# Kernel optimization log

Hardware: AMD Instinct MI355X
Metric: run time of the kernel (lower is better)

## Reference

```python
import jax, jax.numpy as jnp
import numpy as np

B, T, DI, D = 8, 256, 64, 128
PRED_LEN, OUT_DIM = 96, 7
LN_EPS = 1e-5


def setup_inputs() -> dict:
    key = jax.random.key(0)
    ks = jax.random.split(key, 10)
    s = lambda k, shape, sc: (jax.random.normal(k, shape, jnp.float32) * sc)
    return {
        'x': s(ks[0], (B, T, DI), 1.0),
        'W_b': s(ks[1], (DI, D), DI ** -0.5), 'b_b': jnp.zeros((D,), jnp.float32),
        'Wk': s(ks[2], (D, D), D ** -0.5),
        'Wv': s(ks[3], (D, D), D ** -0.5),
        'Wq': s(ks[4], (D, D), D ** -0.5),
        'W_m': s(ks[5], (D, 3), D ** -0.5), 'b_m': jnp.zeros((3,), jnp.float32),
        'W_f': s(ks[6], (2 * D, D), (2 * D) ** -0.5), 'b_f': jnp.zeros((D,), jnp.float32),
        'W1': s(ks[7], (D, D), D ** -0.5), 'b1': jnp.zeros((D,), jnp.float32),
        'g1': jnp.ones((D,), jnp.float32), 'be1': jnp.zeros((D,), jnp.float32),
        'W2': s(ks[8], (D, PRED_LEN * OUT_DIM), D ** -0.5),
        'b2': jnp.zeros((PRED_LEN * OUT_DIM,), jnp.float32),
    }


def _layernorm(h, g, b):
    mu = h.mean(-1, keepdims=True)
    var = jnp.mean((h - mu) ** 2, -1, keepdims=True)
    return (h - mu) * jax.lax.rsqrt(var + LN_EPS) * g + b


def _forward(x, W_b, b_b, Wk, Wv, Wq, W_m, b_m, W_f, b_f, W1, b1, g1, be1, W2, b2):
    # Backbone P: feature extraction -> f_t  [B,T,D]
    f = jax.nn.gelu(x @ W_b + b_b)
    # Meta-learner: per-step (theta_t, eta_t, alpha_t)
    meta = jax.nn.sigmoid(f @ W_m + b_m)               # [B,T,3]
    theta = 0.01 * meta[..., 0]                         # learning rate
    eta = meta[..., 1]                                  # momentum
    alpha = 0.1 * meta[..., 2]                          # forget/decay
    # Key/value/query projections (precomputed; recurrence is in M,S only)
    k = f @ Wk; v = f @ Wv; q = f @ Wq                  # [B,T,D] each
    seq = (jnp.swapaxes(k, 0, 1), jnp.swapaxes(v, 0, 1), jnp.swapaxes(q, 0, 1),
           theta.T, eta.T, alpha.T)                     # time-major
    M0 = jnp.zeros((B, D, D), f.dtype)
    S0 = jnp.zeros((B, D, D), f.dtype)

    def step(carry, inp):
        M, S = carry
        kt, vt, qt, th, et, al = inp
        # grad of 0.5*||M k - v||^2 wrt M  (rank-1 outer product)
        err = jnp.einsum('bij,bj->bi', M, kt) - vt
        grad = jnp.einsum('bi,bj->bij', err, kt)
        S = et[:, None, None] * S - th[:, None, None] * grad
        M = (1.0 - al)[:, None, None] * M + S
        m_t = jnp.einsum('bij,bj->bi', M, qt)           # retrieve
        return (M, S), m_t

    (_, _), m_seq = jax.lax.scan(step, (M0, S0), seq)
    m = jnp.swapaxes(m_seq, 0, 1)                       # [B,T,D]
    # Gated fusion
    gate = jax.nn.sigmoid(jnp.concatenate([f, m], -1) @ W_f + b_f)
    fused = f * gate + m * (1.0 - gate)
    # Prediction head on last timestep (dropout=0 / eval)
    last = fused[:, -1, :]
    h = jax.nn.gelu(_layernorm(last @ W1 + b1, g1, be1))
    out = h @ W2 + b2
    return out.reshape(B, PRED_LEN, OUT_DIM)


def reference(x, W_b, b_b, Wk, Wv, Wq, W_m, b_m, W_f, b_f, W1, b1, g1, be1, W2, b2):
    return _forward(x, W_b, b_b, Wk, Wv, Wq, W_m, b_m, W_f, b_f, W1, b1, g1, be1, W2, b2)
```

## Files before the change

kernel.cpp:

```cpp
#include <hip/hip_runtime.h>
#include <hip/hip_bf16.h>

#define BB 8
#define TT 256
#define DIN 64
#define DD 128

__device__ __forceinline__ float gelu_tanh(float x) {
  float x3 = x * x * x;
  return 0.5f * x * (1.0f + tanhf(0.7978845608028654f * (x + 0.044715f * x3)));
}
__device__ __forceinline__ float sigmoidf(float x) {
  return 1.0f / (1.0f + __expf(-x));
}

template <typename T> __device__ __forceinline__ float getv(const void* p, int i);
template <> __device__ __forceinline__ float getv<float>(const void* p, int i) {
  return ((const float*)p)[i];
}
template <> __device__ __forceinline__ float getv<__hip_bfloat16>(const void* p, int i) {
  return __bfloat162float(((const __hip_bfloat16*)p)[i]);
}

template <int CTRL>
__device__ __forceinline__ float dpp_add(float x) {
  int s = __builtin_amdgcn_update_dpp(0, __float_as_int(x), CTRL, 0xF, 0xF, true);
  return x + __int_as_float(s);
}

__device__ __forceinline__ float rowsum16(float p) {
  p = dpp_add<0xB1>(p);
  p = dpp_add<0x4E>(p);
  p = dpp_add<0x124>(p);
  p = dpp_add<0x128>(p);
  return p;
}

__device__ __forceinline__ void gload_lds16(const void* g, void* l) {
  __builtin_amdgcn_global_load_lds(
      (const __attribute__((address_space(1))) void*)g,
      (__attribute__((address_space(3))) void*)l, 16, 0, 0);
}

__global__ void k0_detect(const void* x, int* flag) {
  __shared__ int cnt;
  if (threadIdx.x == 0) cnt = 0;
  __syncthreads();
  const unsigned short* u = (const unsigned short*)x;
  int good = 0;
  for (int idx = threadIdx.x; idx < 2048; idx += 256) {
    unsigned int bits = ((unsigned int)u[idx]) << 16;
    float f = __uint_as_float(bits);
    float a = fabsf(f);
    if (a == 0.0f || (a > 1e-4f && a < 100.0f)) good++;
  }
  atomicAdd(&cnt, good);
  __syncthreads();
  if (threadIdx.x == 0) *flag = (cnt >= 1536) ? 1 : 0;
}

template <typename T>
__device__ void k1_body(const void* x, const void* W_b, const void* b_b,
                        const void* Wk, const void* Wv, const void* Wq,
                        const void* W_m, const void* b_m,
                        float* kout, float* vout, float* scal4,
                        float* q_last, float* f_last) {
  const int row = blockIdx.x;
  const int b = row >> 8, t = row & 255;
  const int tid = threadIdx.x;
  __shared__ float xs[DIN];
  __shared__ float fs[DD];
  if (tid < DIN) xs[tid] = getv<T>(x, row * DIN + tid);
  __syncthreads();

  float acc = getv<T>(b_b, tid);
#pragma unroll 8
  for (int d = 0; d < DIN; ++d) acc += xs[d] * getv<T>(W_b, d * DD + tid);
  float f = gelu_tanh(acc);
  fs[tid] = f;
  __syncthreads();

  float ak = 0.0f, av = 0.0f;
#pragma unroll 8
  for (int c = 0; c < DD; ++c) {
    float fc = fs[c];
    ak += fc * getv<T>(Wk, c * DD + tid);
    av += fc * getv<T>(Wv, c * DD + tid);
  }
  kout[row * DD + tid] = ak;
  vout[row * DD + tid] = av;

  if (t == TT - 1) {
    float aq = 0.0f;
#pragma unroll 8
    for (int c = 0; c < DD; ++c) aq += fs[c] * getv<T>(Wq, c * DD + tid);
    q_last[b * DD + tid] = aq;
    f_last[b * DD + tid] = f;
  }
  if (tid < 4) {
    float val = 0.0f;
    if (tid < 3) {
      float a = getv<T>(b_m, tid);
      for (int c = 0; c < DD; ++c) a += fs[c] * getv<T>(W_m, c * 3 + tid);
      float s = sigmoidf(a);
      val = (tid == 0) ? 0.01f * s : ((tid == 1) ? s : 0.1f * s);
    }
    scal4[row * 4 + tid] = val;
  }
}

__global__ __launch_bounds__(128) void k1_kern(
    const void* x, const void* W_b, const void* b_b, const void* Wk,
    const void* Wv, const void* Wq, const void* W_m, const void* b_m,
    const int* flag, float* kout, float* vout, float* scal4, float* q_last,
    float* f_last) {
  if (*flag)
    k1_body<__hip_bfloat16>(x, W_b, b_b, Wk, Wv, Wq, W_m, b_m, kout, vout,
                            scal4, q_last, f_last);
  else
    k1_body<float>(x, W_b, b_b, Wk, Wv, Wq, W_m, b_m, kout, vout, scal4,
                   q_last, f_last);
}

__global__ __launch_bounds__(64) void k2_scan(
    const float* __restrict__ kbuf, const float* __restrict__ vbuf,
    const float* __restrict__ scal, const float* __restrict__ q_last,
    float* __restrict__ m_last) {
  const int tid = threadIdx.x;
  const int g = tid & 15;
  const int cidx = tid >> 4;
  const int chain = blockIdx.x * 4 + cidx;
  const int b = chain >> 7;
  const int i = chain & 127;
  const int i0 = (blockIdx.x * 4) & 127;

  __shared__ float kl[2][32 * DD];
  __shared__ float vl[TT * 4];
  __shared__ float4 scl[TT];

  const float* kslice = kbuf + (size_t)b * TT * DD;
  const float* vslice = vbuf + (size_t)b * TT * DD;

  for (int idx = tid; idx < TT * 4; idx += 64)
    vl[idx] = vslice[(idx >> 2) * DD + i0 + (idx & 3)];
  const float4* sp4 = (const float4*)scal + b * TT;
  for (int idx = tid; idx < TT; idx += 64) scl[idx] = sp4[idx];

#define K2_GLL(CH, BUF)                                                      \
  {                                                                          \
    const float* gs = kslice + (CH) * 32 * DD + tid * 4;                     \
    _Pragma("unroll") for (int j = 0; j < 16; ++j)                           \
        gload_lds16(gs + j * 256, &kl[BUF][j * 256]);                        \
  }
  K2_GLL(0, 0);

  float4 Ma = {0, 0, 0, 0}, Mb = {0, 0, 0, 0};
  float4 Sa = {0, 0, 0, 0}, Sb = {0, 0, 0, 0};

#define K2_STEP(KA, KB, VV, SC)                                              \
  {                                                                          \
    float p = (Ma.x * KA.x + Ma.y * KA.y) + (Ma.z * KA.z + Ma.w * KA.w) +    \
              (Mb.x * KB.x + Mb.y * KB.y) + (Mb.z * KB.z + Mb.w * KB.w);     \
    p = rowsum16(p);                                                         \
    const float err = p - VV;                                                \
    const float c = SC.x * err;                             \
    const float et = SC.y;                                          \
    const float am = 1.0f - SC.z;                             \
    Sa.x = et * Sa.x - c * KA.x;  Ma.x = am * Ma.x + Sa.x;                   \
    Sa.y = et * Sa.y - c * KA.y;  Ma.y = am * Ma.y + Sa.y;                   \
    Sa.z = et * Sa.z - c * KA.z;  Ma.z = am * Ma.z + Sa.z;                   \
    Sa.w = et * Sa.w - c * KA.w;  Ma.w = am * Ma.w + Sa.w;                   \
    Sb.x = et * Sb.x - c * KB.x;  Mb.x = am * Mb.x + Sb.x;                   \
    Sb.y = et * Sb.y - c * KB.y;  Mb.y = am * Mb.y + Sb.y;                   \
    Sb.z = et * Sb.z - c * KB.z;  Mb.z = am * Mb.z + Sb.z;                   \
    Sb.w = et * Sb.w - c * KB.w;  Mb.w = am * Mb.w + Sb.w;                   \
  }

  for (int ch = 0; ch < 8; ++ch) {
    asm volatile("s_waitcnt vmcnt(0) lgkmcnt(0)" ::: "memory");
    if (ch < 7) K2_GLL(ch + 1, (ch + 1) & 1);

    const float* kc = &kl[ch & 1][0];
    const int tbase = ch * 32;

    float4 ka = *(const float4*)(kc + g * 8);
    float4 kb = *(const float4*)(kc + g * 8 + 4);
    float vv = vl[tbase * 4 + cidx];
    float4 sc = scl[tbase];

#pragma unroll
    for (int tt = 0; tt < 32; ++tt) {
      float4 nka, nkb, nsc;
      float nv;
      if (tt < 31) {
        nka = *(const float4*)(kc + (tt + 1) * DD + g * 8);
        nkb = *(const float4*)(kc + (tt + 1) * DD + g * 8 + 4);
        nv = vl[(tbase + tt + 1) * 4 + cidx];
        nsc = scl[tbase + tt + 1];
      }
      K2_STEP(ka, kb, vv, sc);
      if (tt < 31) { ka = nka; kb = nkb; vv = nv; sc = nsc; }
    }
  }
#undef K2_STEP
#undef K2_GLL

  const float4* qp = (const float4*)(q_last + b * DD) + (g << 1);
  float4 qa = qp[0], qb = qp[1];
  float p = (Ma.x * qa.x + Ma.y * qa.y) + (Ma.z * qa.z + Ma.w * qa.w) +
            (Mb.x * qb.x + Mb.y * qb.y) + (Mb.z * qb.z + Mb.w * qb.w);
  p = rowsum16(p);
  if (g == 0) m_last[b * DD + i] = p;
}

template <typename T>
__device__ void k3a_body(const float* f_last, const float* m_last,
                         const void* W_f, const void* b_f, const void* W1,
                         const void* b1, const void* g1, const void* be1,
                         float* h_buf) {
  const int b = blockIdx.x, tid = threadIdx.x;
  const int o = tid & 127, s = tid >> 7;
  __shared__ float fm[2 * DD];
  __shared__ float part[1024];
  __shared__ float fused[DD];
  __shared__ float tmp[DD];
  __shared__ float smu, srs;

  if (tid < 2 * DD)
    fm[tid] = (tid < DD) ? f_last[b * DD + tid] : m_last[b * DD + tid - DD];
  __syncthreads();

  {
    float a = 0.0f;
#pragma unroll 8
    for (int cc = 0; cc < 32; ++cc) {
      const int c = s * 32 + cc;
      a += fm[c] * getv<T>(W_f, c * DD + o);
    }
    part[tid] = a;
  }
  __syncthreads();
  if (tid < DD) {
    float a = getv<T>(b_f, tid);
#pragma unroll
    for (int ss = 0; ss < 8; ++ss) a += part[ss * DD + tid];
    float gte = sigmoidf(a);
    fused[tid] = fm[tid] * gte + fm[DD + tid] * (1.0f - gte);
  }
  __syncthreads();

  {
    float a = 0.0f;
#pragma unroll
    for (int cc = 0; cc < 16; ++cc) {
      const int c = s * 16 + cc;
      a += fused[c] * getv<T>(W1, c * DD + o);
    }
    part[tid] = a;
  }
  __syncthreads();
  if (tid < DD) {
    float a = getv<T>(b1, tid);
#pragma unroll
    for (int ss = 0; ss < 8; ++ss) a += part[ss * DD + tid];
    tmp[tid] = a;
  }
  __syncthreads();

  if (tid < 64) {
    float x0 = tmp[tid], x1 = tmp[tid + 64];
    float sm = x0 + x1;
    float sq = x0 * x0 + x1 * x1;
    sm = rowsum16(sm);
    sq = rowsum16(sq);
    sm += __shfl_xor(sm, 16); sq += __shfl_xor(sq, 16);
    sm += __shfl_xor(sm, 32); sq += __shfl_xor(sq, 32);
    if (tid == 0) {
      float mu = sm / (float)DD;
      smu = mu;
      srs = rsqrtf(sq / (float)DD - mu * mu + 1e-5f);
    }
  }
  __syncthreads();

  if (tid < DD)
    h_buf[b * DD + tid] = gelu_tanh((tmp[tid] - smu) * srs * getv<T>(g1, tid) +
                                    getv<T>(be1, tid));
}

__global__ __launch_bounds__(1024) void k3a_kern(
    const float* f_last, const float* m_last, const void* W_f,
    const void* b_f, const void* W1, const void* b1, const void* g1,
    const void* be1, const int* flag, float* h_buf) {
  if (*flag)
    k3a_body<__hip_bfloat16>(f_last, m_last, W_f, b_f, W1, b1, g1, be1, h_buf);
  else
    k3a_body<float>(f_last, m_last, W_f, b_f, W1, b1, g1, be1, h_buf);
}

template <typename T>
__device__ void k3b_body(const float* h_buf, const void* W2, const void* b2,
                         void* out) {
  const int b = blockIdx.x / 11;
  const int jc = blockIdx.x % 11;
  const int tid = threadIdx.x;
  const int j = jc * 64 + (tid & 63);
  const int s = tid >> 6;
  __shared__ float hs[DD];
  __shared__ float part[256];

  if (tid < DD) hs[tid] = h_buf[b * DD + tid];
  __syncthreads();

  float a = 0.0f;
  if (j < 672) {
#pragma unroll 8
    for (int cc = 0; cc < 32; ++cc) {
      const int c = s * 32 + cc;
      a += hs[c] * getv<T>(W2, c * 672 + j);
    }
  }
  part[tid] = a;
  __syncthreads();

  if (tid < 64 && j < 672) {
    float r = part[tid] + part[tid + 64] + part[tid + 128] + part[tid + 192] +
              getv<T>(b2, j);
    if (sizeof(T) == 2)
      ((__hip_bfloat16*)out)[b * 672 + j] = __float2bfloat16(r);
    else
      ((float*)out)[b * 672 + j] = r;
  }
}

__global__ __launch_bounds__(256) void k3b_kern(
    const float* h_buf, const void* W2, const void* b2, const int* flag,
    void* out) {
  if (*flag)
    k3b_body<__hip_bfloat16>(h_buf, W2, b2, out);
  else
    k3b_body<float>(h_buf, W2, b2, out);
}

extern "C" void kernel_launch(void* const* d_in, const int* in_sizes, int n_in,
                              void* d_out, int out_size, void* d_ws,
                              size_t ws_size, hipStream_t stream) {
  const void* x   = d_in[0];
  const void* W_b = d_in[1];
  const void* b_b = d_in[2];
  const void* Wk  = d_in[3];
  const void* Wv  = d_in[4];
  const void* Wq  = d_in[5];
  const void* W_m = d_in[6];
  const void* b_m = d_in[7];
  const void* W_f = d_in[8];
  const void* b_f = d_in[9];
  const void* W1  = d_in[10];
  const void* b1  = d_in[11];
  const void* g1  = d_in[12];
  const void* be1 = d_in[13];
  const void* W2  = d_in[14];
  const void* b2  = d_in[15];

  float* w = (float*)d_ws;
  float* kbuf   = w;
  float* vbuf   = w + 262144;
  float* scal4  = w + 524288;
  float* q_last = w + 532480;
  float* f_last = w + 533504;
  float* m_last = w + 534528;
  int*   flag   = (int*)(w + 535552);
  float* h_buf  = w + 535556;

  k0_detect<<<1, 256, 0, stream>>>(x, flag);
  k1_kern<<<BB * TT, 128, 0, stream>>>(x, W_b, b_b, Wk, Wv, Wq, W_m, b_m,
                                       flag, kbuf, vbuf, scal4, q_last,
                                       f_last);
  k2_scan<<<256, 64, 0, stream>>>(kbuf, vbuf, scal4, q_last, m_last);
  k3a_kern<<<BB, 1024, 0, stream>>>(f_last, m_last, W_f, b_f, W1, b1, g1,
                                    be1, flag, h_buf);
  k3b_kern<<<88, 256, 0, stream>>>(h_buf, W2, b2, flag, d_out);
}
```

Measured before the change: 154.4 us.

## Fuse dtype detection into consumers and merge head kernels into one launch

Drops the separate dtype-detection kernel. Each block of k1 and of the head kernel now repeats the bf16 check itself, reading the first 2048 halfwords of x and summing the counts with a wave reduction. The gated-fusion, LayerNorm and W2 head kernels are merged into one 88-block kernel. Each block recomputes the per-batch gate and LayerNorm path with 256 threads instead of 1024, which removes two launches and the h_buf round trip. The cost is redundant head computation across the 11 blocks per batch and a small extra global read in every k1 block.

After: 153.4 us. Within noise of the previous version (-0.6%).

```diff
diff --git a/kernel.cpp b/kernel.cpp
--- a/kernel.cpp
+++ b/kernel.cpp
@@ -42,21 +42,11 @@
       (__attribute__((address_space(3))) void*)l, 16, 0, 0);
 }
 
-__global__ void k0_detect(const void* x, int* flag) {
-  __shared__ int cnt;
-  if (threadIdx.x == 0) cnt = 0;
-  __syncthreads();
-  const unsigned short* u = (const unsigned short*)x;
-  int good = 0;
-  for (int idx = threadIdx.x; idx < 2048; idx += 256) {
-    unsigned int bits = ((unsigned int)u[idx]) << 16;
-    float f = __uint_as_float(bits);
-    float a = fabsf(f);
-    if (a == 0.0f || (a > 1e-4f && a < 100.0f)) good++;
-  }
-  atomicAdd(&cnt, good);
-  __syncthreads();
-  if (threadIdx.x == 0) *flag = (cnt >= 1536) ? 1 : 0;
+__device__ __forceinline__ int dtype_good(const unsigned short* u, int idx) {
+  unsigned int bits = ((unsigned int)u[idx]) << 16;
+  float f = __uint_as_float(bits);
+  float a = fabsf(f);
+  return (a == 0.0f || (a > 1e-4f && a < 100.0f)) ? 1 : 0;
 }
 
 template <typename T>
@@ -112,9 +102,25 @@
 __global__ __launch_bounds__(128) void k1_kern(
     const void* x, const void* W_b, const void* b_b, const void* Wk,
     const void* Wv, const void* Wq, const void* W_m, const void* b_m,
-    const int* flag, float* kout, float* vout, float* scal4, float* q_last,
-    float* f_last) {
-  if (*flag)
+    float* kout, float* vout, float* scal4, float* q_last, float* f_last) {
+  __shared__ int gcnt[2];
+  {
+    const int tid = threadIdx.x;
+    const unsigned short* u = (const unsigned short*)x;
+    int good = 0;
+#pragma unroll
+    for (int j = 0; j < 16; ++j) good += dtype_good(u, j * 128 + tid);
+    float gf = (float)good;
+    gf = rowsum16(gf);
+    gf += __shfl_xor(gf, 16);
+    gf += __shfl_xor(gf, 32);
+    if ((tid & 63) == 0) gcnt[tid >> 6] = (int)(gf + 0.5f);
+  }
+  __syncthreads();
+  const bool isbf16 = (gcnt[0] + gcnt[1] >= 1536);
+  __syncthreads();
+
+  if (isbf16)
     k1_body<__hip_bfloat16>(x, W_b, b_b, Wk, Wv, Wq, W_m, b_m, kout, vout,
                             scal4, q_last, f_last);
   else
@@ -214,36 +220,36 @@
 }
 
 template <typename T>
-__device__ void k3a_body(const float* f_last, const float* m_last,
-                         const void* W_f, const void* b_f, const void* W1,
-                         const void* b1, const void* g1, const void* be1,
-                         float* h_buf) {
-  const int b = blockIdx.x, tid = threadIdx.x;
+__device__ void k3_body(const float* f_last, const float* m_last,
+                        const void* W_f, const void* b_f, const void* W1,
+                        const void* b1, const void* g1, const void* be1,
+                        const void* W2, const void* b2, void* out) {
+  const int b = blockIdx.x / 11;
+  const int jc = blockIdx.x % 11;
+  const int tid = threadIdx.x;
   const int o = tid & 127, s = tid >> 7;
   __shared__ float fm[2 * DD];
-  __shared__ float part[1024];
+  __shared__ float part[256];
   __shared__ float fused[DD];
   __shared__ float tmp[DD];
+  __shared__ float h[DD];
   __shared__ float smu, srs;
 
-  if (tid < 2 * DD)
-    fm[tid] = (tid < DD) ? f_last[b * DD + tid] : m_last[b * DD + tid - DD];
+  fm[tid] = (tid < DD) ? f_last[b * DD + tid] : m_last[b * DD + tid - DD];
   __syncthreads();
 
   {
     float a = 0.0f;
 #pragma unroll 8
-    for (int cc = 0; cc < 32; ++cc) {
-      const int c = s * 32 + cc;
+    for (int cc = 0; cc < 128; ++cc) {
+      const int c = s * 128 + cc;
       a += fm[c] * getv<T>(W_f, c * DD + o);
     }
     part[tid] = a;
   }
   __syncthreads();
   if (tid < DD) {
-    float a = getv<T>(b_f, tid);
-#pragma unroll
-    for (int ss = 0; ss < 8; ++ss) a += part[ss * DD + tid];
+    float a = getv<T>(b_f, tid) + part[tid] + part[DD + tid];
     float gte = sigmoidf(a);
     fused[tid] = fm[tid] * gte + fm[DD + tid] * (1.0f - gte);
   }
@@ -251,20 +257,15 @@
 
   {
     float a = 0.0f;
-#pragma unroll
-    for (int cc = 0; cc < 16; ++cc) {
-      const int c = s * 16 + cc;
+#pragma unroll 8
+    for (int cc = 0; cc < 64; ++cc) {
+      const int c = s * 64 + cc;
       a += fused[c] * getv<T>(W1, c * DD + o);
     }
     part[tid] = a;
   }
   __syncthreads();
-  if (tid < DD) {
-    float a = getv<T>(b1, tid);
-#pragma unroll
-    for (int ss = 0; ss < 8; ++ss) a += part[ss * DD + tid];
-    tmp[tid] = a;
-  }
+  if (tid < DD) tmp[tid] = getv<T>(b1, tid) + part[tid] + part[DD + tid];
   __syncthreads();
 
   if (tid < 64) {
@@ -284,40 +285,18 @@
   __syncthreads();
 
   if (tid < DD)
-    h_buf[b * DD + tid] = gelu_tanh((tmp[tid] - smu) * srs * getv<T>(g1, tid) +
-                                    getv<T>(be1, tid));
-}
-
-__global__ __launch_bounds__(1024) void k3a_kern(
-    const float* f_last, const float* m_last, const void* W_f,
-    const void* b_f, const void* W1, const void* b1, const void* g1,
-    const void* be1, const int* flag, float* h_buf) {
-  if (*flag)
-    k3a_body<__hip_bfloat16>(f_last, m_last, W_f, b_f, W1, b1, g1, be1, h_buf);
-  else
-    k3a_body<float>(f_last, m_last, W_f, b_f, W1, b1, g1, be1, h_buf);
-}
-
-template <typename T>
-__device__ void k3b_body(const float* h_buf, const void* W2, const void* b2,
-                         void* out) {
-  const int b = blockIdx.x / 11;
-  const int jc = blockIdx.x % 11;
-  const int tid = threadIdx.x;
+    h[tid] = gelu_tanh((tmp[tid] - smu) * srs * getv<T>(g1, tid) +
+                       getv<T>(be1, tid));
+  __syncthreads();
+
   const int j = jc * 64 + (tid & 63);
-  const int s = tid >> 6;
-  __shared__ float hs[DD];
-  __shared__ float part[256];
-
-  if (tid < DD) hs[tid] = h_buf[b * DD + tid];
-  __syncthreads();
-
+  const int s2 = tid >> 6;
   float a = 0.0f;
   if (j < 672) {
 #pragma unroll 8
     for (int cc = 0; cc < 32; ++cc) {
-      const int c = s * 32 + cc;
-      a += hs[c] * getv<T>(W2, c * 672 + j);
+      const int c = s2 * 32 + cc;
+      a += h[c] * getv<T>(W2, c * 672 + j);
     }
   }
   part[tid] = a;
@@ -333,13 +312,32 @@
   }
 }
 
-__global__ __launch_bounds__(256) void k3b_kern(
-    const float* h_buf, const void* W2, const void* b2, const int* flag,
-    void* out) {
-  if (*flag)
-    k3b_body<__hip_bfloat16>(h_buf, W2, b2, out);
+__global__ __launch_bounds__(256) void k3_kern(
+    const void* x, const float* f_last, const float* m_last, const void* W_f,
+    const void* b_f, const void* W1, const void* b1, const void* g1,
+    const void* be1, const void* W2, const void* b2, void* out) {
+  __shared__ int gcnt[4];
+  {
+    const int tid = threadIdx.x;
+    const unsigned short* u = (const unsigned short*)x;
+    int good = 0;
+#pragma unroll
+    for (int j = 0; j < 8; ++j) good += dtype_good(u, j * 256 + tid);
+    float gf = (float)good;
+    gf = rowsum16(gf);
+    gf += __shfl_xor(gf, 16);
+    gf += __shfl_xor(gf, 32);
+    if ((tid & 63) == 0) gcnt[tid >> 6] = (int)(gf + 0.5f);
+  }
+  __syncthreads();
+  const bool isbf16 = (gcnt[0] + gcnt[1] + gcnt[2] + gcnt[3] >= 1536);
+  __syncthreads();
+
+  if (isbf16)
+    k3_body<__hip_bfloat16>(f_last, m_last, W_f, b_f, W1, b1, g1, be1, W2, b2,
+                            out);
   else
-    k3b_body<float>(h_buf, W2, b2, out);
+    k3_body<float>(f_last, m_last, W_f, b_f, W1, b1, g1, be1, W2, b2, out);
 }
 
 extern "C" void kernel_launch(void* const* d_in, const int* in_sizes, int n_in,
@@ -369,15 +367,10 @@
   float* q_last = w + 532480;
   float* f_last = w + 533504;
   float* m_last = w + 534528;
-  int*   flag   = (int*)(w + 535552);
-  float* h_buf  = w + 535556;
-
-  k0_detect<<<1, 256, 0, stream>>>(x, flag);
+
   k1_kern<<<BB * TT, 128, 0, stream>>>(x, W_b, b_b, Wk, Wv, Wq, W_m, b_m,
-                                       flag, kbuf, vbuf, scal4, q_last,
-                                       f_last);
+                                       kbuf, vbuf, scal4, q_last, f_last);
   k2_scan<<<256, 64, 0, stream>>>(kbuf, vbuf, scal4, q_last, m_last);
-  k3a_kern<<<BB, 1024, 0, stream>>>(f_last, m_last, W_f, b_f, W1, b1, g1,
-                                    be1, flag, h_buf);
-  k3b_kern<<<88, 256, 0, stream>>>(h_buf, W2, b2, flag, d_out);
-}
+  k3_kern<<<88, 256, 0, stream>>>(x, f_last, m_last, W_f, b_f, W1, b1, g1,
+                                  be1, W2, b2, d_out);
+}
```
